# Kernel tuning notes

Measured on AMD Instinct MI355X. Metric: run time of the kernel, lower is better.

## Reference

```python
import jax, jax.numpy as jnp
import numpy as np

N_NODES = 50000
N_EDGES = 800000
N_GRAPHS = 64
IN_CH = 128
GLOBAL_DIM = 256
HIDDEN = 64
HEADS = 4
N_CLASSES = 10


def setup_inputs() -> dict:
    key = jax.random.key(0)
    ks = jax.random.split(key, 32)
    lin = lambda k, fi, fo: jax.random.normal(k, (fi, fo), jnp.float32) * 0.02
    inp = {}
    inp["x"] = jax.random.normal(ks[0], (N_NODES, IN_CH), jnp.float32)
    inp["edge_index"] = jax.random.randint(ks[1], (2, N_EDGES), 0, N_NODES)
    inp["batch"] = jnp.sort(jax.random.randint(ks[2], (N_NODES,), 0, N_GRAPHS))
    inp["global_feats"] = jax.random.normal(ks[3], (N_GRAPHS, GLOBAL_DIM), jnp.float32)
    # conv1 (in=IN_CH)
    inp["c1_Wq"] = lin(ks[4], IN_CH, HEADS * HIDDEN); inp["c1_bq"] = jnp.zeros((HEADS * HIDDEN,), jnp.float32)
    inp["c1_Wk"] = lin(ks[5], IN_CH, HEADS * HIDDEN); inp["c1_bk"] = jnp.zeros((HEADS * HIDDEN,), jnp.float32)
    inp["c1_Wv"] = lin(ks[6], IN_CH, HEADS * HIDDEN); inp["c1_bv"] = jnp.zeros((HEADS * HIDDEN,), jnp.float32)
    inp["c1_Ws"] = lin(ks[7], IN_CH, HIDDEN);         inp["c1_bs"] = jnp.zeros((HIDDEN,), jnp.float32)
    # conv2 (in=HIDDEN)
    inp["c2_Wq"] = lin(ks[8], HIDDEN, HEADS * HIDDEN); inp["c2_bq"] = jnp.zeros((HEADS * HIDDEN,), jnp.float32)
    inp["c2_Wk"] = lin(ks[9], HIDDEN, HEADS * HIDDEN); inp["c2_bk"] = jnp.zeros((HEADS * HIDDEN,), jnp.float32)
    inp["c2_Wv"] = lin(ks[10], HIDDEN, HEADS * HIDDEN); inp["c2_bv"] = jnp.zeros((HEADS * HIDDEN,), jnp.float32)
    inp["c2_Ws"] = lin(ks[11], HIDDEN, HIDDEN);         inp["c2_bs"] = jnp.zeros((HIDDEN,), jnp.float32)
    # global MLP
    inp["g_W1"] = lin(ks[12], GLOBAL_DIM, HIDDEN); inp["g_b1"] = jnp.zeros((HIDDEN,), jnp.float32)
    inp["g_W2"] = lin(ks[13], HIDDEN, HIDDEN);     inp["g_b2"] = jnp.zeros((HIDDEN,), jnp.float32)
    # head
    inp["h_W1"] = lin(ks[14], 2 * HIDDEN, HIDDEN); inp["h_b1"] = jnp.zeros((HIDDEN,), jnp.float32)
    inp["h_W2"] = lin(ks[15], HIDDEN, N_CLASSES); inp["h_b2"] = jnp.zeros((N_CLASSES,), jnp.float32)
    return inp


def _tconv(x, src, dst, Wq, bq, Wk, bk, Wv, bv, Ws, bs):
    """PyG TransformerConv, heads=HEADS, concat=False (head-mean), root skip, eval-mode (no dropout)."""
    N = x.shape[0]
    q = (x @ Wq + bq).reshape(N, HEADS, HIDDEN)
    k = (x @ Wk + bk).reshape(N, HEADS, HIDDEN)
    v = (x @ Wv + bv).reshape(N, HEADS, HIDDEN)
    # per-edge attention logits  [E, H]
    s = jnp.einsum('ehd,ehd->eh', q[dst], k[src]) / jnp.sqrt(jnp.float32(HIDDEN))
    # segment softmax over incoming edges of each dst node
    m = jax.ops.segment_max(s, dst, num_segments=N)           # [N, H]
    e = jnp.exp(s - m[dst])                                    # [E, H]
    z = jax.ops.segment_sum(e, dst, num_segments=N)           # [N, H]
    alpha = e / z[dst]                                         # [E, H] (dst always has >=1 edge here)
    agg = jax.ops.segment_sum(alpha[:, :, None] * v[src], dst, num_segments=N)  # [N, H, D]
    return agg.mean(axis=1) + x @ Ws + bs


def reference(x, edge_index, batch, global_feats,
              c1_Wq, c1_bq, c1_Wk, c1_bk, c1_Wv, c1_bv, c1_Ws, c1_bs,
              c2_Wq, c2_bq, c2_Wk, c2_bk, c2_Wv, c2_bv, c2_Ws, c2_bs,
              g_W1, g_b1, g_W2, g_b2, h_W1, h_b1, h_W2, h_b2):
    src, dst = edge_index[0], edge_index[1]
    h = jax.nn.relu(_tconv(x, src, dst, c1_Wq, c1_bq, c1_Wk, c1_bk, c1_Wv, c1_bv, c1_Ws, c1_bs))
    h = jax.nn.relu(_tconv(h, src, dst, c2_Wq, c2_bq, c2_Wk, c2_bk, c2_Wv, c2_bv, c2_Ws, c2_bs))
    # global mean pool per graph
    ssum = jax.ops.segment_sum(h, batch, num_segments=N_GRAPHS)                # [G, HIDDEN]
    cnt = jax.ops.segment_sum(jnp.ones((h.shape[0],), h.dtype), batch, num_segments=N_GRAPHS)
    patch_emb = ssum / jnp.maximum(cnt, 1.0)[:, None]
    g = jax.nn.relu(global_feats @ g_W1 + g_b1)
    g = jax.nn.relu(g @ g_W2 + g_b2)
    fused = jnp.concatenate([patch_emb, g], axis=-1)
    return jax.nn.relu(fused @ h_W1 + h_b1) @ h_W2 + h_b2
```

## Files before the change

kernel.cpp:

```cpp
#include <hip/hip_runtime.h>
#include <hip/hip_bf16.h>
#include <math.h>

#define N_NODES   50000
#define N_EDGES   800000
#define N_GRAPHS  64
#define IN_CH     128
#define GLOBAL_DIM 256
#define HIDDEN    64
#define HEADS     4
#define N_CLASSES 10
#define QKV_COLS  832
#define MAXDEG    64

#define P1B    256
#define EPB    3125
#define NBUCK  196
#define SLABP  48

typedef unsigned short ushort_t;
typedef unsigned int uint_t;
typedef unsigned char uchar_t;
typedef __attribute__((ext_vector_type(8))) short short8;
typedef __attribute__((ext_vector_type(4))) float floatx4;
typedef __attribute__((ext_vector_type(2))) float floatx2;

__device__ __forceinline__ ushort_t bf16rne(float f) {
    uint_t b = __float_as_uint(f);
    b += 0x7fffu + ((b >> 16) & 1u);
    return (ushort_t)(b >> 16);
}
__device__ __forceinline__ float4 bf4_unpack(uint_t lo, uint_t hi) {
    float4 f;
    f.x = __uint_as_float(lo << 16);
    f.y = __uint_as_float(lo & 0xffff0000u);
    f.z = __uint_as_float(hi << 16);
    f.w = __uint_as_float(hi & 0xffff0000u);
    return f;
}
__device__ __forceinline__ uchar_t fp8e4m3(float f) {
    int v = __builtin_amdgcn_cvt_pk_fp8_f32(f, 0.f, 0, false);
    return (uchar_t)(v & 0xff);
}
__device__ __forceinline__ short8 pack_bf8(float4 a, float4 b) {
    union { short8 s; ushort_t u[8]; } r;
    r.u[0] = bf16rne(a.x); r.u[1] = bf16rne(a.y);
    r.u[2] = bf16rne(a.z); r.u[3] = bf16rne(a.w);
    r.u[4] = bf16rne(b.x); r.u[5] = bf16rne(b.y);
    r.u[6] = bf16rne(b.z); r.u[7] = bf16rne(b.w);
    return r.s;
}
__device__ __forceinline__ void graph_range(const int* __restrict__ batch, int g,
                                            int& start, int& end) {
    int lo = 0, hi = N_NODES;
    while (lo < hi) { int mid = (lo + hi) >> 1; if (batch[mid] < g) lo = mid + 1; else hi = mid; }
    start = lo;
    hi = N_NODES;
    while (lo < hi) { int mid = (lo + hi) >> 1; if (batch[mid] < g + 1) lo = mid + 1; else hi = mid; }
    end = lo;
}

#define PREP_CONC_B  624

__global__ __launch_bounds__(256) void prep_p1(
        const float* __restrict__ W1q, const float* __restrict__ W1k,
        const float* __restrict__ W1v, const float* __restrict__ W1s,
        const float* __restrict__ b1q, const float* __restrict__ b1k,
        const float* __restrict__ b1v, const float* __restrict__ b1s,
        const float* __restrict__ W2q, const float* __restrict__ W2k,
        const float* __restrict__ W2v, const float* __restrict__ W2s,
        const float* __restrict__ b2q, const float* __restrict__ b2k,
        const float* __restrict__ b2v, const float* __restrict__ b2s,
        ushort_t* __restrict__ Wt1, ushort_t* __restrict__ Wt2,
        float* __restrict__ bcat1, float* __restrict__ bcat2,
        const int* __restrict__ src, const int* __restrict__ dst,
        uint_t* __restrict__ slab, int* __restrict__ cntm) {
    int b = blockIdx.x, t = threadIdx.x;
    if (b >= PREP_CONC_B) {
        int blk = b - PREP_CONC_B;
        __shared__ int hist[NBUCK];
        for (int i = t; i < NBUCK; i += 256) hist[i] = 0;
        __syncthreads();
        int e0 = blk * EPB;
        int e1 = e0 + EPB;
        for (int e = e0 + t; e < e1; e += 256) {
            int s = src[e], d = dst[e];
            int bu = d >> 8;
            int off = atomicAdd(&hist[bu], 1);
            if (off < SLABP)
                slab[((size_t)bu * P1B + blk) * SLABP + off] =
                    ((uint_t)d << 16) | (uint_t)s;
        }
        __syncthreads();
        for (int i = t; i < NBUCK; i += 256)
            cntm[i * P1B + blk] = hist[i] < SLABP ? hist[i] : SLABP;
        return;
    }
    int idx = b * 256 + t;
    const int T1 = IN_CH * QKV_COLS;
    const int T2 = HIDDEN * QKV_COLS;
    if (idx < T1) {
        int c = idx / IN_CH, k = idx % IN_CH;
        float v;
        if (c < 256)      v = W1q[k * 256 + c];
        else if (c < 512) v = W1k[k * 256 + (c - 256)];
        else if (c < 768) v = W1v[k * 256 + (c - 512)];
        else              v = W1s[k * 64  + (c - 768)];
        Wt1[idx] = bf16rne(v);
    } else if (idx < T1 + T2) {
        int i2 = idx - T1;
        int c = i2 / HIDDEN, k = i2 % HIDDEN;
        float v;
        if (c < 256)      v = W2q[k * 256 + c];
        else if (c < 512) v = W2k[k * 256 + (c - 256)];
        else if (c < 768) v = W2v[k * 256 + (c - 512)];
        else              v = W2s[k * 64  + (c - 768)];
        Wt2[i2] = bf16rne(v);
    }
    if (idx < QKV_COLS) {
        float bb, b2;
        if (idx < 256)      { bb = b1q[idx];       b2 = b2q[idx]; }
        else if (idx < 512) { bb = b1k[idx - 256]; b2 = b2k[idx - 256]; }
        else if (idx < 768) { bb = b1v[idx - 512]; b2 = b2v[idx - 512]; }
        else                { bb = b1s[idx - 768]; b2 = b2s[idx - 768]; }
        bcat1[idx] = bb;
        bcat2[idx] = b2;
    }
}

template <int K, bool A_FP32>
__device__ __forceinline__ void gemm_body11(int idx0, int t,
                                            const void* __restrict__ Av,
                                            const ushort_t* __restrict__ Wt,
                                            const float* __restrict__ bias,
                                            uchar_t* __restrict__ qb8,
                                            uchar_t* __restrict__ kvb,
                                            ushort_t* __restrict__ skipb,
                                            int N, int RB, uchar_t* smem) {
    constexpr int KP = K + 8;
    constexpr int C8 = K / 8;
    ushort_t* Bs = (ushort_t*)smem;

    const int xcd = idx0 & 7;
    const int j = idx0 >> 3;
    const int g = j % 7;
    const int strip = (j / 7) * 8 + xcd;
    if (strip >= RB) return;
    const int base_r = strip * 128;
    const int NC = (g < 6) ? 128 : 64;
    const int base_c = (g < 6) ? g * 128 : 768;

#pragma unroll
    for (int i = 0; i < (128 * C8) / 256; ++i) {
        int ii = t + i * 256;
        int n = ii / C8, c = ii % C8;
        if (n < NC)
            *(uint4*)(Bs + n * KP + c * 8) =
                *(const uint4*)(Wt + (size_t)(base_c + n) * K + c * 8);
    }

    const int wave = t >> 6, lane = t & 63;
    const int quad = lane >> 4, m16 = lane & 15;

    int arow0 = base_r + wave * 32 + m16;
    int arow1 = arow0 + 16;
    int cr0 = arow0 < N ? arow0 : N - 1;
    int cr1 = arow1 < N ? arow1 : N - 1;
    short8 a0[K / 32], a1[K / 32];
    if (A_FP32) {
        const float* A = (const float*)Av;
        const float* Ar0 = A + (size_t)cr0 * K + quad * 8;
        const float* Ar1 = A + (size_t)cr1 * K + quad * 8;
#pragma unroll
        for (int kc = 0; kc < K / 32; ++kc) {
            float4 f0 = *(const float4*)(Ar0 + kc * 32);
            float4 f1 = *(const float4*)(Ar0 + kc * 32 + 4);
            a0[kc] = pack_bf8(f0, f1);
            float4 g0 = *(const float4*)(Ar1 + kc * 32);
            float4 g1 = *(const float4*)(Ar1 + kc * 32 + 4);
            a1[kc] = pack_bf8(g0, g1);
        }
    } else {
        const ushort_t* A = (const ushort_t*)Av;
        const ushort_t* Ar0 = A + (size_t)cr0 * K + quad * 8;
        const ushort_t* Ar1 = A + (size_t)cr1 * K + quad * 8;
#pragma unroll
        for (int kc = 0; kc < K / 32; ++kc) {
            a0[kc] = *(const short8*)(Ar0 + kc * 32);
            a1[kc] = *(const short8*)(Ar1 + kc * 32);
        }
    }
    __syncthreads();

    if (g < 6) {
        floatx4 acc[2][8];
#pragma unroll
        for (int rt = 0; rt < 2; ++rt)
#pragma unroll
            for (int c2 = 0; c2 < 8; ++c2) acc[rt][c2] = (floatx4){0.f, 0.f, 0.f, 0.f};
#pragma unroll
        for (int kc = 0; kc < K / 32; ++kc) {
            int ko = kc * 32 + quad * 8;
#pragma unroll
            for (int c2 = 0; c2 < 8; ++c2) {
                short8 b = *(const short8*)(Bs + (c2 * 16 + m16) * KP + ko);
                acc[0][c2] = __builtin_amdgcn_mfma_f32_16x16x32_bf16(a0[kc], b, acc[0][c2], 0, 0, 0);
                acc[1][c2] = __builtin_amdgcn_mfma_f32_16x16x32_bf16(a1[kc], b, acc[1][c2], 0, 0, 0);
            }
        }
        float bb[8];
#pragma unroll
        for (int c2 = 0; c2 < 8; ++c2) bb[c2] = bias[base_c + c2 * 16 + m16];
#pragma unroll
        for (int rt = 0; rt < 2; ++rt)
#pragma unroll
            for (int c2 = 0; c2 < 8; ++c2)
#pragma unroll
                for (int r = 0; r < 4; ++r) acc[rt][c2][r] += bb[c2];

        __syncthreads();

        uchar_t* ep = smem;
#pragma unroll
        for (int c2 = 0; c2 < 8; ++c2) {
            int col_l = c2 * 16 + m16;
#pragma unroll
            for (int rt = 0; rt < 2; ++rt)
#pragma unroll
                for (int r = 0; r < 4; ++r)
                    ep[(wave * 32 + rt * 16 + quad * 4 + r) * 144 + col_l] =
                        fp8e4m3(acc[rt][c2][r]);
        }
        __syncthreads();
        if (g < 2) {
#pragma unroll
            for (int i = 0; i < 4; ++i) {
                int ii = t + i * 256;
                int row = ii >> 3, ch = ii & 7;
                int gr = base_r + row;
                if (gr < N)
                    *(uint4*)(qb8 + (size_t)gr * 256 + g * 128 + ch * 16) =
                        *(const uint4*)(ep + row * 144 + ch * 16);
            }
        } else {
            const int half = (g & 1);
            const int vo = (g >= 4) ? 8 : 0;
#pragma unroll
            for (int i = 0; i < 8; ++i) {
                int ii = t + i * 256;
                int row = ii >> 4, ch = ii & 15;
                int gr = base_r + row;
                if (gr < N)
                    *(uint2*)(kvb + (size_t)gr * 512 + half * 256 + ch * 16 + vo) =
                        *(const uint2*)(ep + row * 144 + ch * 8);
            }
        }
    } else {
        floatx4 acc[2][4];
#pragma unroll
        for (int rt = 0; rt < 2; ++rt)
#pragma unroll
            for (int c2 = 0; c2 < 4; ++c2) acc[rt][c2] = (floatx4){0.f, 0.f, 0.f, 0.f};
#pragma unroll
        for (int kc = 0; kc < K / 32; ++kc) {
            int ko = kc * 32 + quad * 8;
#pragma unroll
            for (int c2 = 0; c2 < 4; ++c2) {
                short8 b = *(const short8*)(Bs + (c2 * 16 + m16) * KP + ko);
                acc[0][c2] = __builtin_amdgcn_mfma_f32_16x16x32_bf16(a0[kc], b, acc[0][c2], 0, 0, 0);
                acc[1][c2] = __builtin_amdgcn_mfma_f32_16x16x32_bf16(a1[kc], b, acc[1][c2], 0, 0, 0);
            }
        }
        float bb[4];
#pragma unroll
        for (int c2 = 0; c2 < 4; ++c2) bb[c2] = bias[768 + c2 * 16 + m16];
#pragma unroll
        for (int rt = 0; rt < 2; ++rt)
#pragma unroll
            for (int c2 = 0; c2 < 4; ++c2)
#pragma unroll
                for (int r = 0; r < 4; ++r) acc[rt][c2][r] += bb[c2];

        __syncthreads();

        ushort_t* ep = (ushort_t*)smem;
#pragma unroll
        for (int c2 = 0; c2 < 4; ++c2) {
            int col_l = c2 * 16 + m16;
#pragma unroll
            for (int rt = 0; rt < 2; ++rt)
#pragma unroll
                for (int r = 0; r < 4; ++r)
                    ep[(wave * 32 + rt * 16 + quad * 4 + r) * 68 + col_l] =
                        bf16rne(acc[rt][c2][r]);
        }
        __syncthreads();
#pragma unroll
        for (int i = 0; i < 4; ++i) {
            int ii = t + i * 256;
            int row = ii >> 3, ch = ii & 7;
            int gr = base_r + row;
            if (gr < N)
                *(uint4*)(skipb + (size_t)gr * 64 + ch * 8) =
                    *(const uint4*)(ep + row * 68 + ch * 8);
        }
    }
}

template <int K, bool A_FP32>
__global__ __launch_bounds__(256) void gemm_fill9(const void* __restrict__ Av,
                                                  const ushort_t* __restrict__ Wt,
                                                  const float* __restrict__ bias,
                                                  uchar_t* __restrict__ qb8,
                                                  uchar_t* __restrict__ kvb,
                                                  ushort_t* __restrict__ skipb,
                                                  int N, int RB,
                                                  const int* __restrict__ cntm,
                                                  const uint_t* __restrict__ slab,
                                                  int* __restrict__ deg,
                                                  ushort_t* __restrict__ col) {
    __shared__ uchar_t smem[(K == 128) ? 34816 : 18432] __attribute__((aligned(16)));
    int t = threadIdx.x;
    int idx = (int)blockIdx.x;
    if (idx < NBUCK) {
        __shared__ int cnt2[256];
        __shared__ int cs[P1B];
        if (t < P1B) cs[t] = cntm[idx * P1B + t];
        cnt2[t] = 0;
        __syncthreads();
        const uint_t* myslab = slab + (size_t)idx * P1B * SLABP;
        for (int i = t; i < P1B * SLABP; i += 256) {
            int blkq = i / SLABP;
            int off = i - blkq * SLABP;
            if (off < cs[blkq]) {
                uint_t rec = myslab[i];
                int d = rec >> 16;
                int pos = atomicAdd(&cnt2[d & 255], 1);
                col[((size_t)d << 6) + pos] = (ushort_t)(rec & 0xffffu);
            }
        }
        __syncthreads();
        int gn = (idx << 8) + t;
        if (gn < N_NODES) deg[gn] = cnt2[t];
        return;
    }
    gemm_body11<K, A_FP32>(idx - NBUCK, t, Av, Wt, bias, qb8, kvb, skipb, N, RB, smem);
}

template <int K, bool A_FP32>
__global__ __launch_bounds__(256) void gemm_v9(const void* __restrict__ Av,
                                               const ushort_t* __restrict__ Wt,
                                               const float* __restrict__ bias,
                                               uchar_t* __restrict__ qb8,
                                               uchar_t* __restrict__ kvb,
                                               ushort_t* __restrict__ skipb,
                                               int N, int RB) {
    __shared__ uchar_t smem[(K == 128) ? 34816 : 18432] __attribute__((aligned(16)));
    gemm_body11<K, A_FP32>((int)blockIdx.x, threadIdx.x, Av, Wt, bias,
                           qb8, kvb, skipb, N, RB, smem);
}

__device__ __forceinline__ void edge_step3(uint2 k8, uint2 v8, const floatx2* qp,
                                           float& z, floatx2* acp) {
    floatx2 dp = qp[0] * __builtin_amdgcn_cvt_pk_f32_fp8(k8.x, false);
    dp += qp[1] * __builtin_amdgcn_cvt_pk_f32_fp8(k8.x, true);
    dp += qp[2] * __builtin_amdgcn_cvt_pk_f32_fp8(k8.y, false);
    dp += qp[3] * __builtin_amdgcn_cvt_pk_f32_fp8(k8.y, true);
    float d = dp[0] + dp[1];
    d += __shfl_xor(d, 1);
    d += __shfl_xor(d, 2);
    d += __shfl_xor(d, 4);
    float p = __expf(d);
    z += p;
    floatx2 pp = {p, p};
    acp[0] += pp * __builtin_amdgcn_cvt_pk_f32_fp8(v8.x, false);
    acp[1] += pp * __builtin_amdgcn_cvt_pk_f32_fp8(v8.x, true);
    acp[2] += pp * __builtin_amdgcn_cvt_pk_f32_fp8(v8.y, false);
    acp[3] += pp * __builtin_amdgcn_cvt_pk_f32_fp8(v8.y, true);
}

template <bool OUT_BF16>
__global__ __launch_bounds__(256) void attn_agg7(const uchar_t* __restrict__ qb8,
                                                 const uchar_t* __restrict__ kvb,
                                                 const ushort_t* __restrict__ skipb,
                                                 const int* __restrict__ deg,
                                                 const ushort_t* __restrict__ col,
                                                 void* __restrict__ hout) {
    int node = blockIdx.x * 4 + threadIdx.y;
    if (node >= N_NODES) return;
    int lane = threadIdx.x;
    int half = lane >> 5, sl = lane & 31;
    uint2 qd = *(const uint2*)(qb8 + (size_t)node * 256 + sl * 8);
    const floatx2 s8 = {0.125f, 0.125f};
    floatx2 qp[4];
    qp[0] = s8 * __builtin_amdgcn_cvt_pk_f32_fp8(qd.x, false);
    qp[1] = s8 * __builtin_amdgcn_cvt_pk_f32_fp8(qd.x, true);
    qp[2] = s8 * __builtin_amdgcn_cvt_pk_f32_fp8(qd.y, false);
    qp[3] = s8 * __builtin_amdgcn_cvt_pk_f32_fp8(qd.y, true);
    floatx2 acp[4];
    acp[0] = (floatx2){0.f, 0.f}; acp[1] = (floatx2){0.f, 0.f};
    acp[2] = (floatx2){0.f, 0.f}; acp[3] = (floatx2){0.f, 0.f};
    float z = 0.f;
    int dv = deg[node];
    int creg = (int)col[(node << 6) | lane];
    int e = half;
    const uchar_t* kb = kvb + (size_t)sl * 16;
    for (; e + 6 < dv; e += 8) {
        int c0 = __shfl(creg, e);
        int c1 = __shfl(creg, e + 2);
        int c2 = __shfl(creg, e + 4);
        int c3 = __shfl(creg, e + 6);
        uint4 x0 = *(const uint4*)(kb + (size_t)c0 * 512);
        uint4 x1 = *(const uint4*)(kb + (size_t)c1 * 512);
        uint4 x2 = *(const uint4*)(kb + (size_t)c2 * 512);
        uint4 x3 = *(const uint4*)(kb + (size_t)c3 * 512);
        edge_step3(make_uint2(x0.x, x0.y), make_uint2(x0.z, x0.w), qp, z, acp);
        edge_step3(make_uint2(x1.x, x1.y), make_uint2(x1.z, x1.w), qp, z, acp);
        edge_step3(make_uint2(x2.x, x2.y), make_uint2(x2.z, x2.w), qp, z, acp);
        edge_step3(make_uint2(x3.x, x3.y), make_uint2(x3.z, x3.w), qp, z, acp);
    }
    for (; e < dv; e += 2) {
        int c0 = __shfl(creg, e);
        uint4 x0 = *(const uint4*)(kb + (size_t)c0 * 512);
        edge_step3(make_uint2(x0.x, x0.y), make_uint2(x0.z, x0.w), qp, z, acp);
    }
    z += __shfl_xor(z, 32);
    float ac[8] = {acp[0][0], acp[0][1], acp[1][0], acp[1][1],
                   acp[2][0], acp[2][1], acp[3][0], acp[3][1]};
#pragma unroll
    for (int i = 0; i < 8; ++i) ac[i] += __shfl_xor(ac[i], 32);
    float inv = (z > 0.f) ? (0.25f / z) : 0.f;
#pragma unroll
    for (int i = 0; i < 8; ++i) ac[i] *= inv;
#pragma unroll
    for (int i = 0; i < 8; ++i) {
        ac[i] += __shfl_xor(ac[i], 8);
        ac[i] += __shfl_xor(ac[i], 16);
    }
    if (lane < 8) {
        uint4 su = *(const uint4*)(skipb + (size_t)node * 64 + lane * 8);
        float4 s0 = bf4_unpack(su.x, su.y);
        float4 s1 = bf4_unpack(su.z, su.w);
        float o0 = fmaxf(ac[0] + s0.x, 0.f);
        float o1 = fmaxf(ac[1] + s0.y, 0.f);
        float o2 = fmaxf(ac[2] + s0.z, 0.f);
        float o3 = fmaxf(ac[3] + s0.w, 0.f);
        float o4 = fmaxf(ac[4] + s1.x, 0.f);
        float o5 = fmaxf(ac[5] + s1.y, 0.f);
        float o6 = fmaxf(ac[6] + s1.z, 0.f);
        float o7 = fmaxf(ac[7] + s1.w, 0.f);
        if (OUT_BF16) {
            uint4 u;
            u.x = (uint_t)bf16rne(o0) | ((uint_t)bf16rne(o1) << 16);
            u.y = (uint_t)bf16rne(o2) | ((uint_t)bf16rne(o3) << 16);
            u.z = (uint_t)bf16rne(o4) | ((uint_t)bf16rne(o5) << 16);
            u.w = (uint_t)bf16rne(o6) | ((uint_t)bf16rne(o7) << 16);
            *(uint4*)((ushort_t*)hout + (size_t)node * HIDDEN + lane * 8) = u;
        } else {
            float* op = (float*)hout + (size_t)node * HIDDEN + lane * 8;
            *(float4*)(op)     = make_float4(o0, o1, o2, o3);
            *(float4*)(op + 4) = make_float4(o4, o5, o6, o7);
        }
    }
}

__global__ __launch_bounds__(256) void pool_partial(const float* __restrict__ h,
                                                    const int* __restrict__ batch,
                                                    float* __restrict__ part) {
    int g = blockIdx.x >> 3;
    int s = blockIdx.x & 7;
    int start, end;
    graph_range(batch, g, start, end);
    int len = end - start;
    int s0 = start + (len * s) / 8;
    int s1 = start + (len * (s + 1)) / 8;
    int t = threadIdx.x;
    int d = t & 63, chunk = t >> 6;
    float acc = 0.f;
    for (int n = s0 + chunk; n < s1; n += 4) acc += h[(size_t)n * HIDDEN + d];
    __shared__ float sh[256];
    sh[t] = acc;
    __syncthreads();
    if (t < 64)
        part[(size_t)blockIdx.x * 64 + t] = sh[t] + sh[64 + t] + sh[128 + t] + sh[192 + t];
}

__global__ __launch_bounds__(256) void head_mlp(const float* __restrict__ part,
                                                const int* __restrict__ batch,
                                                const float* __restrict__ gf,
                                                const float* __restrict__ gW1, const float* __restrict__ gb1,
                                                const float* __restrict__ gW2, const float* __restrict__ gb2,
                                                const float* __restrict__ hW1, const float* __restrict__ hb1,
                                                const float* __restrict__ hW2, const float* __restrict__ hb2,
                                                float* __restrict__ out) {
    int g = blockIdx.x;
    int t = threadIdx.x;
    int d = t & 63, kk = t >> 6;
    int start, end;
    graph_range(batch, g, start, end);
    float cnt = fmaxf((float)(end - start), 1.0f);
    __shared__ float gfs[GLOBAL_DIM];
    __shared__ float fused[2 * HIDDEN];
    __shared__ float g1[HIDDEN];
    __shared__ float h1s[HIDDEN];
    __shared__ float red[256];
    gfs[t] = gf[(size_t)g * GLOBAL_DIM + t];
    if (t < 64) {
        float s = 0.f;
#pragma unroll
        for (int i = 0; i < 8; ++i) s += part[((size_t)g * 8 + i) * 64 + t];
        fused[t] = s / cnt;
    }
    __syncthreads();
    {
        float a = 0.f;
        int k0 = kk * 64;
#pragma unroll 4
        for (int k = k0; k < k0 + 64; ++k) a = fmaf(gfs[k], gW1[k * HIDDEN + d], a);
        red[t] = a;
        __syncthreads();
        if (t < 64) g1[t] = fmaxf(red[t] + red[64 + t] + red[128 + t] + red[192 + t] + gb1[t], 0.f);
        __syncthreads();
    }
    {
        float a = 0.f;
        int k0 = kk * 16;
#pragma unroll 4
        for (int k = k0; k < k0 + 16; ++k) a = fmaf(g1[k], gW2[k * HIDDEN + d], a);
        red[t] = a;
        __syncthreads();
        if (t < 64) fused[HIDDEN + t] =
            fmaxf(red[t] + red[64 + t] + red[128 + t] + red[192 + t] + gb2[t], 0.f);
        __syncthreads();
    }
    {
        float a = 0.f;
        int k0 = kk * 32;
#pragma unroll 4
        for (int k = k0; k < k0 + 32; ++k) a = fmaf(fused[k], hW1[k * HIDDEN + d], a);
        red[t] = a;
        __syncthreads();
        if (t < 64) h1s[t] = fmaxf(red[t] + red[64 + t] + red[128 + t] + red[192 + t] + hb1[t], 0.f);
        __syncthreads();
    }
    if (t < N_CLASSES) {
        float o = hb2[t];
#pragma unroll 4
        for (int k = 0; k < HIDDEN; ++k) o = fmaf(h1s[k], hW2[k * N_CLASSES + t], o);
        out[(size_t)g * N_CLASSES + t] = o;
    }
}

extern "C" void kernel_launch(void* const* d_in, const int* in_sizes, int n_in,
                              void* d_out, int out_size, void* d_ws, size_t ws_size,
                              hipStream_t stream) {
    const float* x        = (const float*)d_in[0];
    const int*   eidx     = (const int*)d_in[1];
    const int*   batch    = (const int*)d_in[2];
    const float* gfeats   = (const float*)d_in[3];
    const float* c1_Wq = (const float*)d_in[4];  const float* c1_bq = (const float*)d_in[5];
    const float* c1_Wk = (const float*)d_in[6];  const float* c1_bk = (const float*)d_in[7];
    const float* c1_Wv = (const float*)d_in[8];  const float* c1_bv = (const float*)d_in[9];
    const float* c1_Ws = (const float*)d_in[10]; const float* c1_bs = (const float*)d_in[11];
    const float* c2_Wq = (const float*)d_in[12]; const float* c2_bq = (const float*)d_in[13];
    const float* c2_Wk = (const float*)d_in[14]; const float* c2_bk = (const float*)d_in[15];
    const float* c2_Wv = (const float*)d_in[16]; const float* c2_bv = (const float*)d_in[17];
    const float* c2_Ws = (const float*)d_in[18]; const float* c2_bs = (const float*)d_in[19];
    const float* g_W1 = (const float*)d_in[20]; const float* g_b1 = (const float*)d_in[21];
    const float* g_W2 = (const float*)d_in[22]; const float* g_b2 = (const float*)d_in[23];
    const float* h_W1 = (const float*)d_in[24]; const float* h_b1 = (const float*)d_in[25];
    const float* h_W2 = (const float*)d_in[26]; const float* h_b2 = (const float*)d_in[27];
    float* out = (float*)d_out;

    const int* srcp = eidx;
    const int* dstp = eidx + N_EDGES;

    char* base = (char*)d_ws;
    uchar_t*  kvb  = (uchar_t*)base;  base += (size_t)N_NODES * 512;
    uchar_t*  qb8  = (uchar_t*)base;  base += (size_t)N_NODES * 256;
    ushort_t* skipb = (ushort_t*)base; base += (size_t)N_NODES * HIDDEN * 2;
    ushort_t* h1b  = (ushort_t*)base; base += (size_t)N_NODES * HIDDEN * 2;
    float*    h2   = (float*)base;    base += (size_t)N_NODES * HIDDEN * 4;
    ushort_t* Wt1  = (ushort_t*)base; base += (size_t)IN_CH * QKV_COLS * 2;
    ushort_t* Wt2  = (ushort_t*)base; base += (size_t)HIDDEN * QKV_COLS * 2;
    float*    bcat1 = (float*)base;   base += QKV_COLS * 4;
    float*    bcat2 = (float*)base;   base += QKV_COLS * 4;
    float*    part = (float*)base;    base += (size_t)N_GRAPHS * 8 * 64 * 4;
    int*      deg  = (int*)base;      base += (size_t)N_NODES * 4;
    ushort_t* colb = (ushort_t*)base; base += ((size_t)N_NODES * MAXDEG + 64) * 2;

    uint_t* slab = (uint_t*)h2;
    int*    cntm = (int*)((char*)h2 + (size_t)NBUCK * P1B * SLABP * 4);

    const int RB = (N_NODES + 127) / 128;
    const int GG = 8 * 7 * ((RB + 7) / 8);
    dim3 attn_block(64, 4);
    int attn_grid = (N_NODES + 3) / 4;

    prep_p1<<<PREP_CONC_B + P1B, 256, 0, stream>>>(
        c1_Wq, c1_Wk, c1_Wv, c1_Ws, c1_bq, c1_bk, c1_bv, c1_bs,
        c2_Wq, c2_Wk, c2_Wv, c2_Ws, c2_bq, c2_bk, c2_bv, c2_bs,
        Wt1, Wt2, bcat1, bcat2, srcp, dstp, slab, cntm);

    gemm_fill9<IN_CH, true><<<NBUCK + GG, 256, 0, stream>>>(
        x, Wt1, bcat1, qb8, kvb, skipb, N_NODES, RB, cntm, slab, deg, colb);
    attn_agg7<true><<<attn_grid, attn_block, 0, stream>>>(qb8, kvb, skipb, deg, colb, h1b);

    gemm_v9<HIDDEN, false><<<GG, 256, 0, stream>>>(h1b, Wt2, bcat2, qb8, kvb, skipb, N_NODES, RB);
    attn_agg7<false><<<attn_grid, attn_block, 0, stream>>>(qb8, kvb, skipb, deg, colb, h2);

    pool_partial<<<N_GRAPHS * 8, 256, 0, stream>>>(h2, batch, part);
    head_mlp<<<N_GRAPHS, 256, 0, stream>>>(part, batch, gfeats,
                                           g_W1, g_b1, g_W2, g_b2,
                                           h_W1, h_b1, h_W2, h_b2, out);
}
```

Before: 343.2 us.

## Pre-convert x to bf16 in prep kernel and halve GEMM row tile to 64

Adds extra blocks to the prep kernel that convert the fp32 input features to bf16 in a workspace buffer, so the first GEMM reads bf16 directly. The GEMM row tile shrinks from 128 to 64 rows per block (one 16-row MFMA tile per wave), which doubles the grid. For K=128 the weight tile is staged through shared memory in two 64-column halves, roughly halving LDS use. The aim is more occupancy and parallelism and less register pressure. The costs are an extra round trip through memory for the bf16 copy of x, weight tiles loaded twice as often across blocks, and an extra barrier.

```diff
diff --git a/kernel.cpp b/kernel.cpp
--- a/kernel.cpp
+++ b/kernel.cpp
@@ -17,6 +17,8 @@
 #define EPB    3125
 #define NBUCK  196
 #define SLABP  48
+
+#define XCB    3125
 
 typedef unsigned short ushort_t;
 typedef unsigned int uint_t;
@@ -74,8 +76,16 @@
         ushort_t* __restrict__ Wt1, ushort_t* __restrict__ Wt2,
         float* __restrict__ bcat1, float* __restrict__ bcat2,
         const int* __restrict__ src, const int* __restrict__ dst,
-        uint_t* __restrict__ slab, int* __restrict__ cntm) {
+        uint_t* __restrict__ slab, int* __restrict__ cntm,
+        const float* __restrict__ x, ushort_t* __restrict__ xb) {
     int b = blockIdx.x, t = threadIdx.x;
+    if (b >= PREP_CONC_B + P1B) {
+        int base = (b - (PREP_CONC_B + P1B)) * 2048 + t * 8;
+        float4 f0 = *(const float4*)(x + base);
+        float4 f1 = *(const float4*)(x + base + 4);
+        *(short8*)(xb + base) = pack_bf8(f0, f1);
+        return;
+    }
     if (b >= PREP_CONC_B) {
         int blk = b - PREP_CONC_B;
         __shared__ int hist[NBUCK];
@@ -128,9 +138,9 @@
     }
 }
 
-template <int K, bool A_FP32>
-__device__ __forceinline__ void gemm_body11(int idx0, int t,
-                                            const void* __restrict__ Av,
+template <int K>
+__device__ __forceinline__ void gemm_body12(int idx0, int t,
+                                            const ushort_t* __restrict__ A,
                                             const ushort_t* __restrict__ Wt,
                                             const float* __restrict__ bias,
                                             uchar_t* __restrict__ qb8,
@@ -146,95 +156,87 @@
     const int g = j % 7;
     const int strip = (j / 7) * 8 + xcd;
     if (strip >= RB) return;
-    const int base_r = strip * 128;
-    const int NC = (g < 6) ? 128 : 64;
-    const int base_c = (g < 6) ? g * 128 : 768;
-
-#pragma unroll
-    for (int i = 0; i < (128 * C8) / 256; ++i) {
-        int ii = t + i * 256;
-        int n = ii / C8, c = ii % C8;
-        if (n < NC)
-            *(uint4*)(Bs + n * KP + c * 8) =
-                *(const uint4*)(Wt + (size_t)(base_c + n) * K + c * 8);
-    }
+    const int base_r = strip * 64;
 
     const int wave = t >> 6, lane = t & 63;
     const int quad = lane >> 4, m16 = lane & 15;
 
-    int arow0 = base_r + wave * 32 + m16;
-    int arow1 = arow0 + 16;
-    int cr0 = arow0 < N ? arow0 : N - 1;
-    int cr1 = arow1 < N ? arow1 : N - 1;
-    short8 a0[K / 32], a1[K / 32];
-    if (A_FP32) {
-        const float* A = (const float*)Av;
-        const float* Ar0 = A + (size_t)cr0 * K + quad * 8;
-        const float* Ar1 = A + (size_t)cr1 * K + quad * 8;
-#pragma unroll
-        for (int kc = 0; kc < K / 32; ++kc) {
-            float4 f0 = *(const float4*)(Ar0 + kc * 32);
-            float4 f1 = *(const float4*)(Ar0 + kc * 32 + 4);
-            a0[kc] = pack_bf8(f0, f1);
-            float4 g0 = *(const float4*)(Ar1 + kc * 32);
-            float4 g1 = *(const float4*)(Ar1 + kc * 32 + 4);
-            a1[kc] = pack_bf8(g0, g1);
-        }
-    } else {
-        const ushort_t* A = (const ushort_t*)Av;
-        const ushort_t* Ar0 = A + (size_t)cr0 * K + quad * 8;
-        const ushort_t* Ar1 = A + (size_t)cr1 * K + quad * 8;
-#pragma unroll
-        for (int kc = 0; kc < K / 32; ++kc) {
-            a0[kc] = *(const short8*)(Ar0 + kc * 32);
-            a1[kc] = *(const short8*)(Ar1 + kc * 32);
-        }
-    }
-    __syncthreads();
+    int arow = base_r + wave * 16 + m16;
+    int cr = arow < N ? arow : N - 1;
+    const ushort_t* Ar = A + (size_t)cr * K + quad * 8;
+    short8 a[K / 32];
+#pragma unroll
+    for (int kc = 0; kc < K / 32; ++kc) a[kc] = *(const short8*)(Ar + kc * 32);
 
     if (g < 6) {
-        floatx4 acc[2][8];
-#pragma unroll
-        for (int rt = 0; rt < 2; ++rt)
-#pragma unroll
-            for (int c2 = 0; c2 < 8; ++c2) acc[rt][c2] = (floatx4){0.f, 0.f, 0.f, 0.f};
-#pragma unroll
-        for (int kc = 0; kc < K / 32; ++kc) {
-            int ko = kc * 32 + quad * 8;
-#pragma unroll
-            for (int c2 = 0; c2 < 8; ++c2) {
-                short8 b = *(const short8*)(Bs + (c2 * 16 + m16) * KP + ko);
-                acc[0][c2] = __builtin_amdgcn_mfma_f32_16x16x32_bf16(a0[kc], b, acc[0][c2], 0, 0, 0);
-                acc[1][c2] = __builtin_amdgcn_mfma_f32_16x16x32_bf16(a1[kc], b, acc[1][c2], 0, 0, 0);
+        const int base_c = g * 128;
+        floatx4 acc[8];
+#pragma unroll
+        for (int c2 = 0; c2 < 8; ++c2) acc[c2] = (floatx4){0.f, 0.f, 0.f, 0.f};
+
+        if (K == 128) {
+#pragma unroll
+            for (int hc = 0; hc < 2; ++hc) {
+                if (hc) __syncthreads();
+#pragma unroll
+                for (int i = 0; i < 4; ++i) {
+                    int ii = t + i * 256;
+                    int n = ii / C8, c = ii % C8;
+                    *(uint4*)(Bs + n * KP + c * 8) =
+                        *(const uint4*)(Wt + (size_t)(base_c + hc * 64 + n) * K + c * 8);
+                }
+                __syncthreads();
+#pragma unroll
+                for (int kc = 0; kc < K / 32; ++kc) {
+                    int ko = kc * 32 + quad * 8;
+#pragma unroll
+                    for (int c2 = 0; c2 < 4; ++c2) {
+                        short8 b = *(const short8*)(Bs + (c2 * 16 + m16) * KP + ko);
+                        acc[hc * 4 + c2] =
+                            __builtin_amdgcn_mfma_f32_16x16x32_bf16(a[kc], b, acc[hc * 4 + c2], 0, 0, 0);
+                    }
+                }
             }
-        }
-        float bb[8];
-#pragma unroll
-        for (int c2 = 0; c2 < 8; ++c2) bb[c2] = bias[base_c + c2 * 16 + m16];
-#pragma unroll
-        for (int rt = 0; rt < 2; ++rt)
-#pragma unroll
-            for (int c2 = 0; c2 < 8; ++c2)
-#pragma unroll
-                for (int r = 0; r < 4; ++r) acc[rt][c2][r] += bb[c2];
-
-        __syncthreads();
-
+        } else {
+#pragma unroll
+            for (int i = 0; i < 4; ++i) {
+                int ii = t + i * 256;
+                int n = ii / C8, c = ii % C8;
+                *(uint4*)(Bs + n * KP + c * 8) =
+                    *(const uint4*)(Wt + (size_t)(base_c + n) * K + c * 8);
+            }
+            __syncthreads();
+#pragma unroll
+            for (int kc = 0; kc < K / 32; ++kc) {
+                int ko = kc * 32 + quad * 8;
+#pragma unroll
+                for (int c2 = 0; c2 < 8; ++c2) {
+                    short8 b = *(const short8*)(Bs + (c2 * 16 + m16) * KP + ko);
+                    acc[c2] = __builtin_amdgcn_mfma_f32_16x16x32_bf16(a[kc], b, acc[c2], 0, 0, 0);
+                }
+            }
+        }
+
+#pragma unroll
+        for (int c2 = 0; c2 < 8; ++c2) {
+            float bb = bias[base_c + c2 * 16 + m16];
+#pragma unroll
+            for (int r = 0; r < 4; ++r) acc[c2][r] += bb;
+        }
+
+        __syncthreads();
         uchar_t* ep = smem;
 #pragma unroll
         for (int c2 = 0; c2 < 8; ++c2) {
             int col_l = c2 * 16 + m16;
 #pragma unroll
-            for (int rt = 0; rt < 2; ++rt)
-#pragma unroll
-                for (int r = 0; r < 4; ++r)
-                    ep[(wave * 32 + rt * 16 + quad * 4 + r) * 144 + col_l] =
-                        fp8e4m3(acc[rt][c2][r]);
+            for (int r = 0; r < 4; ++r)
+                ep[(wave * 16 + quad * 4 + r) * 144 + col_l] = fp8e4m3(acc[c2][r]);
         }
         __syncthreads();
         if (g < 2) {
 #pragma unroll
-            for (int i = 0; i < 4; ++i) {
+            for (int i = 0; i < 2; ++i) {
                 int ii = t + i * 256;
                 int row = ii >> 3, ch = ii & 7;
                 int gr = base_r + row;
@@ -246,7 +248,7 @@
             const int half = (g & 1);
             const int vo = (g >= 4) ? 8 : 0;
 #pragma unroll
-            for (int i = 0; i < 8; ++i) {
+            for (int i = 0; i < 4; ++i) {
                 int ii = t + i * 256;
                 int row = ii >> 4, ch = ii & 15;
                 int gr = base_r + row;
@@ -256,70 +258,68 @@
             }
         }
     } else {
-        floatx4 acc[2][4];
-#pragma unroll
-        for (int rt = 0; rt < 2; ++rt)
-#pragma unroll
-            for (int c2 = 0; c2 < 4; ++c2) acc[rt][c2] = (floatx4){0.f, 0.f, 0.f, 0.f};
+        floatx4 acc[4];
+#pragma unroll
+        for (int c2 = 0; c2 < 4; ++c2) acc[c2] = (floatx4){0.f, 0.f, 0.f, 0.f};
+        constexpr int NU4 = (64 * C8) / 256;
+#pragma unroll
+        for (int i = 0; i < NU4; ++i) {
+            int ii = t + i * 256;
+            int n = ii / C8, c = ii % C8;
+            *(uint4*)(Bs + n * KP + c * 8) =
+                *(const uint4*)(Wt + (size_t)(768 + n) * K + c * 8);
+        }
+        __syncthreads();
 #pragma unroll
         for (int kc = 0; kc < K / 32; ++kc) {
             int ko = kc * 32 + quad * 8;
 #pragma unroll
             for (int c2 = 0; c2 < 4; ++c2) {
                 short8 b = *(const short8*)(Bs + (c2 * 16 + m16) * KP + ko);
-                acc[0][c2] = __builtin_amdgcn_mfma_f32_16x16x32_bf16(a0[kc], b, acc[0][c2], 0, 0, 0);
-                acc[1][c2] = __builtin_amdgcn_mfma_f32_16x16x32_bf16(a1[kc], b, acc[1][c2], 0, 0, 0);
+                acc[c2] = __builtin_amdgcn_mfma_f32_16x16x32_bf16(a[kc], b, acc[c2], 0, 0, 0);
             }
         }
-        float bb[4];
-#pragma unroll
-        for (int c2 = 0; c2 < 4; ++c2) bb[c2] = bias[768 + c2 * 16 + m16];
-#pragma unroll
-        for (int rt = 0; rt < 2; ++rt)
-#pragma unroll
-            for (int c2 = 0; c2 < 4; ++c2)
-#pragma unroll
-                for (int r = 0; r < 4; ++r) acc[rt][c2][r] += bb[c2];
-
-        __syncthreads();
-
+#pragma unroll
+        for (int c2 = 0; c2 < 4; ++c2) {
+            float bb = bias[768 + c2 * 16 + m16];
+#pragma unroll
+            for (int r = 0; r < 4; ++r) acc[c2][r] += bb;
+        }
+        __syncthreads();
         ushort_t* ep = (ushort_t*)smem;
 #pragma unroll
         for (int c2 = 0; c2 < 4; ++c2) {
             int col_l = c2 * 16 + m16;
 #pragma unroll
-            for (int rt = 0; rt < 2; ++rt)
-#pragma unroll
-                for (int r = 0; r < 4; ++r)
-                    ep[(wave * 32 + rt * 16 + quad * 4 + r) * 68 + col_l] =
-                        bf16rne(acc[rt][c2][r]);
-        }
-        __syncthreads();
-#pragma unroll
-        for (int i = 0; i < 4; ++i) {
+            for (int r = 0; r < 4; ++r)
+                ep[(wave * 16 + quad * 4 + r) * 72 + col_l] = bf16rne(acc[c2][r]);
+        }
+        __syncthreads();
+#pragma unroll
+        for (int i = 0; i < 2; ++i) {
             int ii = t + i * 256;
             int row = ii >> 3, ch = ii & 7;
             int gr = base_r + row;
             if (gr < N)
                 *(uint4*)(skipb + (size_t)gr * 64 + ch * 8) =
-                    *(const uint4*)(ep + row * 68 + ch * 8);
-        }
-    }
-}
-
-template <int K, bool A_FP32>
-__global__ __launch_bounds__(256) void gemm_fill9(const void* __restrict__ Av,
-                                                  const ushort_t* __restrict__ Wt,
-                                                  const float* __restrict__ bias,
-                                                  uchar_t* __restrict__ qb8,
-                                                  uchar_t* __restrict__ kvb,
-                                                  ushort_t* __restrict__ skipb,
-                                                  int N, int RB,
-                                                  const int* __restrict__ cntm,
-                                                  const uint_t* __restrict__ slab,
-                                                  int* __restrict__ deg,
-                                                  ushort_t* __restrict__ col) {
-    __shared__ uchar_t smem[(K == 128) ? 34816 : 18432] __attribute__((aligned(16)));
+                    *(const uint4*)(ep + row * 72 + ch * 8);
+        }
+    }
+}
+
+template <int K>
+__global__ __launch_bounds__(256) void gemm_fill12(const ushort_t* __restrict__ A,
+                                                   const ushort_t* __restrict__ Wt,
+                                                   const float* __restrict__ bias,
+                                                   uchar_t* __restrict__ qb8,
+                                                   uchar_t* __restrict__ kvb,
+                                                   ushort_t* __restrict__ skipb,
+                                                   int N, int RB,
+                                                   const int* __restrict__ cntm,
+                                                   const uint_t* __restrict__ slab,
+                                                   int* __restrict__ deg,
+                                                   ushort_t* __restrict__ col) {
+    __shared__ uchar_t smem[(K == 128) ? 17408 : 18432] __attribute__((aligned(16)));
     int t = threadIdx.x;
     int idx = (int)blockIdx.x;
     if (idx < NBUCK) {
@@ -344,20 +344,20 @@
         if (gn < N_NODES) deg[gn] = cnt2[t];
         return;
     }
-    gemm_body11<K, A_FP32>(idx - NBUCK, t, Av, Wt, bias, qb8, kvb, skipb, N, RB, smem);
-}
-
-template <int K, bool A_FP32>
-__global__ __launch_bounds__(256) void gemm_v9(const void* __restrict__ Av,
-                                               const ushort_t* __restrict__ Wt,
-                                               const float* __restrict__ bias,
-                                               uchar_t* __restrict__ qb8,
-                                               uchar_t* __restrict__ kvb,
-                                               ushort_t* __restrict__ skipb,
-                                               int N, int RB) {
-    __shared__ uchar_t smem[(K == 128) ? 34816 : 18432] __attribute__((aligned(16)));
-    gemm_body11<K, A_FP32>((int)blockIdx.x, threadIdx.x, Av, Wt, bias,
-                           qb8, kvb, skipb, N, RB, smem);
+    gemm_body12<K>(idx - NBUCK, t, A, Wt, bias, qb8, kvb, skipb, N, RB, smem);
+}
+
+template <int K>
+__global__ __launch_bounds__(256) void gemm_v12(const ushort_t* __restrict__ A,
+                                                const ushort_t* __restrict__ Wt,
+                                                const float* __restrict__ bias,
+                                                uchar_t* __restrict__ qb8,
+                                                uchar_t* __restrict__ kvb,
+                                                ushort_t* __restrict__ skipb,
+                                                int N, int RB) {
+    __shared__ uchar_t smem[(K == 128) ? 17408 : 18432] __attribute__((aligned(16)));
+    gemm_body12<K>((int)blockIdx.x, threadIdx.x, A, Wt, bias,
+                   qb8, kvb, skipb, N, RB, smem);
 }
 
 __device__ __forceinline__ void edge_step3(uint2 k8, uint2 v8, const floatx2* qp,
@@ -588,25 +588,26 @@
     float*    part = (float*)base;    base += (size_t)N_GRAPHS * 8 * 64 * 4;
     int*      deg  = (int*)base;      base += (size_t)N_NODES * 4;
     ushort_t* colb = (ushort_t*)base; base += ((size_t)N_NODES * MAXDEG + 64) * 2;
+    ushort_t* xb   = (ushort_t*)base; base += (size_t)N_NODES * IN_CH * 2;
 
     uint_t* slab = (uint_t*)h2;
     int*    cntm = (int*)((char*)h2 + (size_t)NBUCK * P1B * SLABP * 4);
 
-    const int RB = (N_NODES + 127) / 128;
+    const int RB = (N_NODES + 63) / 64;
     const int GG = 8 * 7 * ((RB + 7) / 8);
     dim3 attn_block(64, 4);
     int attn_grid = (N_NODES + 3) / 4;
 
-    prep_p1<<<PREP_CONC_B + P1B, 256, 0, stream>>>(
+    prep_p1<<<PREP_CONC_B + P1B + XCB, 256, 0, stream>>>(
         c1_Wq, c1_Wk, c1_Wv, c1_Ws, c1_bq, c1_bk, c1_bv, c1_bs,
         c2_Wq, c2_Wk, c2_Wv, c2_Ws, c2_bq, c2_bk, c2_bv, c2_bs,
-        Wt1, Wt2, bcat1, bcat2, srcp, dstp, slab, cntm);
-
-    gemm_fill9<IN_CH, true><<<NBUCK + GG, 256, 0, stream>>>(
-        x, Wt1, bcat1, qb8, kvb, skipb, N_NODES, RB, cntm, slab, deg, colb);
+        Wt1, Wt2, bcat1, bcat2, srcp, dstp, slab, cntm, x, xb);
+
+    gemm_fill12<IN_CH><<<NBUCK + GG, 256, 0, stream>>>(
+        xb, Wt1, bcat1, qb8, kvb, skipb, N_NODES, RB, cntm, slab, deg, colb);
     attn_agg7<true><<<attn_grid, attn_block, 0, stream>>>(qb8, kvb, skipb, deg, colb, h1b);
 
-    gemm_v9<HIDDEN, false><<<GG, 256, 0, stream>>>(h1b, Wt2, bcat2, qb8, kvb, skipb, N_NODES, RB);
+    gemm_v12<HIDDEN><<<GG, 256, 0, stream>>>(h1b, Wt2, bcat2, qb8, kvb, skipb, N_NODES, RB);
     attn_agg7<false><<<attn_grid, attn_block, 0, stream>>>(qb8, kvb, skipb, deg, colb, h2);
 
     pool_partial<<<N_GRAPHS * 8, 256, 0, stream>>>(h2, batch, part);
```

New measurement: 331.4 us (median of 2 runs). 1.04x faster.
